# Performance work log

Measured on AMD Instinct MI355X. Metric: run time of the kernel, lower is better.

The kernel has to match this reference:

```python
import jax, jax.numpy as jnp
import numpy as np

N, E, D, L, G = 10000, 320000, 256, 5, 128
RWSE, DEG_V = 16, 1001
BN_EPS = 1e-5


def setup_inputs() -> dict:
    key = jax.random.key(0)
    ks = jax.random.split(key, 12)
    s = 1.0 / np.sqrt(D)
    return {
        'feat_id': jax.random.randint(ks[0], (N,), 0, 100000, dtype=jnp.int64 if jax.config.jax_enable_x64 else jnp.int32),
        'edge_index': jax.random.randint(ks[1], (2, E), 0, N),
        'batch_idx': jnp.sort(jax.random.randint(ks[2], (N,), 0, G)),
        'rwse': jax.random.normal(ks[3], (N, RWSE), jnp.float32),
        'in_degrees': jax.random.randint(ks[4], (N,), 0, DEG_V),
        # value_projection: Linear(fixed_input_dim=D -> D); stored as [in, out]
        'w_val': jax.random.normal(ks[5], (D, D), jnp.float32) * s,
        'b_val': jnp.zeros((D,), jnp.float32),
        # rwse_projection: Linear(RWSE -> D)
        'w_rwse': jax.random.normal(ks[6], (RWSE, D), jnp.float32) * (1.0 / np.sqrt(RWSE)),
        'b_rwse': jnp.zeros((D,), jnp.float32),
        # degree_embedding table (clamped to [0, 1000])
        'deg_emb': jax.random.normal(ks[7], (DEG_V, D), jnp.float32) * 0.02,
        # per-layer GIN MLP: Linear-ReLU-Linear, stacked over L layers
        'mlp_w1': jax.random.normal(ks[8], (L, D, D), jnp.float32) * s,
        'mlp_b1': jnp.zeros((L, D), jnp.float32),
        'mlp_w2': jax.random.normal(ks[9], (L, D, D), jnp.float32) * s,
        'mlp_b2': jnp.zeros((L, D), jnp.float32),
        # BatchNorm1d (eval mode: running stats)
        'bn_gamma': jnp.ones((L, D), jnp.float32),
        'bn_beta': jnp.zeros((L, D), jnp.float32),
        'bn_mean': jnp.zeros((L, D), jnp.float32),
        'bn_var': jax.random.uniform(ks[10], (L, D), jnp.float32, 0.5, 1.5),
        # GIN eps per layer
        'eps_gin': jnp.zeros((L,), jnp.float32),
    }


def reference(feat_id, edge_index, batch_idx, rwse, in_degrees,
              w_val, b_val, w_rwse, b_rwse, deg_emb,
              mlp_w1, mlp_b1, mlp_w2, mlp_b2,
              bn_gamma, bn_beta, bn_mean, bn_var, eps_gin):
    # --- node feature embedding ---
    h_id = jnp.remainder(feat_id, D)
    h_one = jax.nn.one_hot(h_id, D, dtype=jnp.float32)            # [N, D]
    h = h_one @ w_val + b_val + rwse @ w_rwse + b_rwse            # value + rwse projections
    deg = jnp.clip(in_degrees, 0, 1000)
    h = h + deg_emb[deg]                                          # degree embedding

    src, dst = edge_index[0], edge_index[1]
    for l in range(L):
        # GIN message passing: sum neighbor features into dst (gather -> scatter-add)
        agg = jax.ops.segment_sum(h[src], dst, num_segments=N)    # [N, D]
        y = agg + (1.0 + eps_gin[l]) * h
        # MLP (Linear-ReLU-Linear)
        y = jax.nn.relu(y @ mlp_w1[l] + mlp_b1[l]) @ mlp_w2[l] + mlp_b2[l]
        # BatchNorm1d (eval: running stats) + ReLU
        y = (y - bn_mean[l]) * (bn_gamma[l] * jax.lax.rsqrt(bn_var[l] + BN_EPS)) + bn_beta[l]
        h = jax.nn.relu(y)

    # --- mean pooling per graph ---
    sums = jax.ops.segment_sum(h, batch_idx, num_segments=G)                     # [G, D]
    cnt = jax.ops.segment_sum(jnp.ones((N, 1), h.dtype), batch_idx, num_segments=G)
    graph_feature = sums / jnp.maximum(cnt, 1.0)
    return graph_feature, h
```

## Files before the change

kernel.cpp:

```cpp
#include <hip/hip_runtime.h>
#include <hip/hip_bf16.h>

#define N_NODES 10000
#define N_EDGES 320000
#define DIM     256
#define N_LAYERS 5
#define N_GRAPHS 128
#define RWSE_K  16
#define GBM 16

typedef __bf16 bf16_t;
typedef bf16_t bf16x8 __attribute__((ext_vector_type(8)));
typedef float  f32x4  __attribute__((ext_vector_type(4)));

__device__ inline ushort f2bf(float f) {
    union { float f; unsigned u; } v; v.f = f;
    unsigned r = v.u + 0x7fff + ((v.u >> 16) & 1);
    return (ushort)(r >> 16);
}
__device__ inline float bfbits2f(unsigned hi16) {
    union { unsigned u; float f; } v; v.u = hi16;
    return v.f;
}

__global__ __launch_bounds__(256)
void setup_kernel(const int* __restrict__ feat_id,
                  const float* __restrict__ rwse,
                  const int* __restrict__ in_deg,
                  const float* __restrict__ w_val,
                  const float* __restrict__ b_val,
                  const float* __restrict__ w_rwse,
                  const float* __restrict__ b_rwse,
                  const float* __restrict__ deg_emb,
                  ushort* __restrict__ hb,
                  const int* __restrict__ ei, int* __restrict__ cnt_arr,
                  const float* __restrict__ w1, const float* __restrict__ w2,
                  ushort* __restrict__ wt1, ushort* __restrict__ wt2,
                  const float* __restrict__ gamma, const float* __restrict__ beta,
                  const float* __restrict__ mean, const float* __restrict__ var,
                  const float* __restrict__ b2, float* __restrict__ scale,
                  float* __restrict__ shift) {
    __shared__ float r[RWSE_K];
    __shared__ float t[32][33];
    int b = blockIdx.x;
    int tid = threadIdx.x;
    if (b < N_NODES) {
        int i = b, d = tid;
        if (d < RWSE_K) r[d] = rwse[i * RWSE_K + d];
        __syncthreads();
        int hid = feat_id[i] & (DIM - 1);
        int dg = in_deg[i];
        dg = dg < 0 ? 0 : (dg > 1000 ? 1000 : dg);
        float v = w_val[hid * DIM + d] + b_val[d] + b_rwse[d] + deg_emb[dg * DIM + d];
#pragma unroll
        for (int k = 0; k < RWSE_K; ++k) v += r[k] * w_rwse[k * DIM + d];
        hb[i * DIM + d] = f2bf(v);
    } else if (b < 11250) {
        int e = (b - N_NODES) * 256 + tid;
        if (e < N_EDGES) atomicAdd(&cnt_arr[ei[N_EDGES + e]], 1);
    } else if (b < 11890) {
        int w_id = b - 11250;
        int l = w_id >> 7;
        int rem = w_id & 127;
        int mat = rem >> 6;
        int tile = rem & 63;
        const float* W  = (mat ? w2  : w1)  + (size_t)l * DIM * DIM;
        ushort*      Wt = (mat ? wt2 : wt1) + (size_t)l * DIM * DIM;
        int k0 = (tile >> 3) * 32, n0 = (tile & 7) * 32;
        int tx = tid & 31, ty = tid >> 5;
#pragma unroll
        for (int j = 0; j < 4; ++j)
            t[ty + j * 8][tx] = W[(k0 + ty + j * 8) * DIM + n0 + tx];
        __syncthreads();
#pragma unroll
        for (int j = 0; j < 4; ++j)
            Wt[(n0 + ty + j * 8) * DIM + k0 + tx] = f2bf(t[tx][ty + j * 8]);
    } else {
        int l = b - 11890;
        int idx = l * DIM + tid;
        float s = gamma[idx] * rsqrtf(var[idx] + 1e-5f);
        scale[idx] = s;
        shift[idx] = beta[idx] + (b2[idx] - mean[idx]) * s;
    }
}

__global__ __launch_bounds__(1024)
void scan_kernel(const int* __restrict__ cnt_arr, int* __restrict__ cur, int n) {
    __shared__ int wsum[16];
    __shared__ int carry_sh;
    int tid = threadIdx.x, wave = tid >> 6, lane = tid & 63;
    if (tid == 0) carry_sh = 0;
    __syncthreads();
    for (int base = 0; base < n; base += 1024) {
        int idx = base + tid;
        int v = (idx < n) ? cnt_arr[idx] : 0;
        int s = v;
#pragma unroll
        for (int off = 1; off < 64; off <<= 1) {
            int t = __shfl_up(s, off, 64);
            if (lane >= off) s += t;
        }
        if (lane == 63) wsum[wave] = s;
        __syncthreads();
        if (wave == 0) {
            int ws = (lane < 16) ? wsum[lane] : 0;
#pragma unroll
            for (int off = 1; off < 16; off <<= 1) {
                int t = __shfl_up(ws, off, 64);
                if (lane >= off) ws += t;
            }
            if (lane < 16) wsum[lane] = ws;
        }
        __syncthreads();
        int excl = s - v + (wave ? wsum[wave - 1] : 0) + carry_sh;
        if (idx < n) cur[idx] = excl;
        __syncthreads();
        if (tid == 0) carry_sh += wsum[15];
        __syncthreads();
    }
}

__global__ __launch_bounds__(256)
void fill_kernel(const int* __restrict__ ei, int* __restrict__ cur,
                 int* __restrict__ cs) {
    int e = blockIdx.x * 256 + threadIdx.x;
    if (e < N_EDGES) {
        int d = ei[N_EDGES + e];
        int p = atomicAdd(&cur[d], 1);
        cs[p] = ei[e];
    }
}

#define ACCV(v)                                                        \
    acc[0] += bfbits2f((v).x << 16); acc[1] += bfbits2f((v).x & 0xffff0000u); \
    acc[2] += bfbits2f((v).y << 16); acc[3] += bfbits2f((v).y & 0xffff0000u); \
    acc[4] += bfbits2f((v).z << 16); acc[5] += bfbits2f((v).z & 0xffff0000u); \
    acc[6] += bfbits2f((v).w << 16); acc[7] += bfbits2f((v).w & 0xffff0000u);

__global__ __launch_bounds__(256)
void agg_kernel(const ushort* __restrict__ hb,
                const int* __restrict__ cur, const int* __restrict__ cs,
                const float* __restrict__ eps_gin, int layer,
                ushort* __restrict__ y) {
    int wave = threadIdx.x >> 6;
    int lane = threadIdx.x & 63;
    int half = lane >> 5;
    int sl   = lane & 31;
    int i = blockIdx.x * 4 + wave;
    if (i >= N_NODES) return;
    const uint4* hb4 = (const uint4*)hb;
    float acc[8];
#pragma unroll
    for (int t = 0; t < 8; ++t) acc[t] = 0.f;

    int e0 = i ? cur[i - 1] : 0;
    int e1 = cur[i];
    for (int base = e0; base < e1; base += 64) {
        int rem = e1 - base;
        int cnt = rem < 64 ? rem : 64;
        int idx = (base + lane < e1) ? cs[base + lane] : 0;
        int j = 0;
        for (; j + 8 <= cnt; j += 8) {
            int s0 = __shfl(idx, j + half, 64);
            int s1 = __shfl(idx, j + 2 + half, 64);
            int s2 = __shfl(idx, j + 4 + half, 64);
            int s3 = __shfl(idx, j + 6 + half, 64);
            uint4 v0 = hb4[(size_t)s0 * 32 + sl];
            uint4 v1 = hb4[(size_t)s1 * 32 + sl];
            uint4 v2 = hb4[(size_t)s2 * 32 + sl];
            uint4 v3 = hb4[(size_t)s3 * 32 + sl];
            ACCV(v0); ACCV(v1); ACCV(v2); ACCV(v3);
        }
        for (; j + 2 <= cnt; j += 2) {
            int s = __shfl(idx, j + half, 64);
            uint4 v = hb4[(size_t)s * 32 + sl];
            ACCV(v);
        }
        if (j < cnt) {
            int s = __shfl(idx, j, 64);
            if (half == 0) {
                uint4 v = hb4[(size_t)s * 32 + sl];
                ACCV(v);
            }
        }
    }
#pragma unroll
    for (int t = 0; t < 8; ++t) acc[t] += __shfl_xor(acc[t], 32, 64);
    if (half == 0) {
        float sc = 1.0f + eps_gin[layer];
        uint4 sv = hb4[(size_t)i * 32 + sl];
        acc[0] += bfbits2f(sv.x << 16) * sc; acc[1] += bfbits2f(sv.x & 0xffff0000u) * sc;
        acc[2] += bfbits2f(sv.y << 16) * sc; acc[3] += bfbits2f(sv.y & 0xffff0000u) * sc;
        acc[4] += bfbits2f(sv.z << 16) * sc; acc[5] += bfbits2f(sv.z & 0xffff0000u) * sc;
        acc[6] += bfbits2f(sv.w << 16) * sc; acc[7] += bfbits2f(sv.w & 0xffff0000u) * sc;
        uint4 o;
        o.x = (uint)f2bf(acc[0]) | ((uint)f2bf(acc[1]) << 16);
        o.y = (uint)f2bf(acc[2]) | ((uint)f2bf(acc[3]) << 16);
        o.z = (uint)f2bf(acc[4]) | ((uint)f2bf(acc[5]) << 16);
        o.w = (uint)f2bf(acc[6]) | ((uint)f2bf(acc[7]) << 16);
        ((uint4*)y)[(size_t)i * 32 + sl] = o;
    }
}

__global__ __launch_bounds__(256)
void gemm12_kernel(const ushort* __restrict__ A, const ushort* __restrict__ Wt1,
                   const float* __restrict__ b1, const ushort* __restrict__ Wt2,
                   const float* __restrict__ bnsc, const float* __restrict__ bnsh,
                   float* __restrict__ outF, ushort* __restrict__ outB, int nrows) {
    __shared__ __align__(16) ushort As[GBM][40];
    __shared__ __align__(16) ushort Bs[DIM][40];
    __shared__ __align__(16) ushort Ts[GBM][DIM + 8];
    int tx = threadIdx.x;
    int row0 = blockIdx.x * GBM;
    int wave = tx >> 6, lane = tx & 63, quad = lane >> 4, l16 = lane & 15;
    int wc = wave * 64;
    int srow = tx >> 2;
    int skol = (tx & 3) * 8;

    f32x4 acc[4];
#pragma unroll
    for (int t = 0; t < 4; ++t) acc[t] = (f32x4){0.f, 0.f, 0.f, 0.f};

    for (int k0 = 0; k0 < DIM; k0 += 32) {
        if (tx < 64) {
            int arow = row0 + srow;
            uint4 av = make_uint4(0u, 0u, 0u, 0u);
            if (arow < nrows) av = *(const uint4*)&A[(size_t)arow * DIM + k0 + skol];
            *(uint4*)&As[srow][skol] = av;
        }
#pragma unroll
        for (int j = 0; j < 4; ++j) {
            int r = srow + 64 * j;
            *(uint4*)&Bs[r][skol] = *(const uint4*)&Wt1[(size_t)r * DIM + k0 + skol];
        }
        __syncthreads();
        bf16x8 af = *(const bf16x8*)&As[l16][quad * 8];
#pragma unroll
        for (int tj = 0; tj < 4; ++tj) {
            bf16x8 bf = *(const bf16x8*)&Bs[wc + tj * 16 + l16][quad * 8];
            acc[tj] = __builtin_amdgcn_mfma_f32_16x16x32_bf16(af, bf, acc[tj], 0, 0, 0);
        }
        __syncthreads();
    }
#pragma unroll
    for (int tj = 0; tj < 4; ++tj) {
        int col = wc + tj * 16 + l16;
        float bias = b1[col];
#pragma unroll
        for (int r = 0; r < 4; ++r)
            Ts[quad * 4 + r][col] = f2bf(fmaxf(acc[tj][r] + bias, 0.f));
    }
    __syncthreads();

#pragma unroll
    for (int t = 0; t < 4; ++t) acc[t] = (f32x4){0.f, 0.f, 0.f, 0.f};
    for (int k0 = 0; k0 < DIM; k0 += 32) {
#pragma unroll
        for (int j = 0; j < 4; ++j) {
            int r = srow + 64 * j;
            *(uint4*)&Bs[r][skol] = *(const uint4*)&Wt2[(size_t)r * DIM + k0 + skol];
        }
        __syncthreads();
        bf16x8 af = *(const bf16x8*)&Ts[l16][k0 + quad * 8];
#pragma unroll
        for (int tj = 0; tj < 4; ++tj) {
            bf16x8 bf = *(const bf16x8*)&Bs[wc + tj * 16 + l16][quad * 8];
            acc[tj] = __builtin_amdgcn_mfma_f32_16x16x32_bf16(af, bf, acc[tj], 0, 0, 0);
        }
        __syncthreads();
    }
#pragma unroll
    for (int tj = 0; tj < 4; ++tj) {
        int col = wc + tj * 16 + l16;
        float s = bnsc[col], sh = bnsh[col];
#pragma unroll
        for (int r = 0; r < 4; ++r) {
            int row = row0 + quad * 4 + r;
            if (row < nrows) {
                float v = fmaxf(acc[tj][r] * s + sh, 0.f);
                if (outF) outF[(size_t)row * DIM + col] = v;
                if (outB) outB[(size_t)row * DIM + col] = f2bf(v);
            }
        }
    }
}

__global__ __launch_bounds__(256)
void pool_kernel(const float* __restrict__ hfin, const int* __restrict__ batch,
                 float* __restrict__ out) {
    int g = blockIdx.x;
    int d = threadIdx.x;
    int l = 0, r = N_NODES;
    while (l < r) { int m = (l + r) >> 1; if (batch[m] < g) l = m + 1; else r = m; }
    int lo = l;
    r = N_NODES;
    while (l < r) { int m = (l + r) >> 1; if (batch[m] < g + 1) l = m + 1; else r = m; }
    int hi = l;
    float a0 = 0.f, a1 = 0.f, a2 = 0.f, a3 = 0.f;
    int i = lo;
    for (; i + 4 <= hi; i += 4) {
        a0 += hfin[(size_t)i * DIM + d];
        a1 += hfin[(size_t)(i + 1) * DIM + d];
        a2 += hfin[(size_t)(i + 2) * DIM + d];
        a3 += hfin[(size_t)(i + 3) * DIM + d];
    }
    for (; i < hi; ++i) a0 += hfin[(size_t)i * DIM + d];
    float c = (float)(hi - lo);
    if (c < 1.f) c = 1.f;
    out[g * DIM + d] = ((a0 + a1) + (a2 + a3)) / c;
}

extern "C" void kernel_launch(void* const* d_in, const int* in_sizes, int n_in,
                              void* d_out, int out_size, void* d_ws, size_t ws_size,
                              hipStream_t stream) {
    const int*   feat_id  = (const int*)d_in[0];
    const int*   ei       = (const int*)d_in[1];
    const int*   batch    = (const int*)d_in[2];
    const float* rwse     = (const float*)d_in[3];
    const int*   in_deg   = (const int*)d_in[4];
    const float* w_val    = (const float*)d_in[5];
    const float* b_val    = (const float*)d_in[6];
    const float* w_rwse   = (const float*)d_in[7];
    const float* b_rwse   = (const float*)d_in[8];
    const float* deg_emb  = (const float*)d_in[9];
    const float* mlp_w1   = (const float*)d_in[10];
    const float* mlp_b1   = (const float*)d_in[11];
    const float* mlp_w2   = (const float*)d_in[12];
    const float* mlp_b2   = (const float*)d_in[13];
    const float* bn_gamma = (const float*)d_in[14];
    const float* bn_beta  = (const float*)d_in[15];
    const float* bn_mean  = (const float*)d_in[16];
    const float* bn_var   = (const float*)d_in[17];
    const float* eps_gin  = (const float*)d_in[18];

    float* out = (float*)d_out;
    float* out_h = out + N_GRAPHS * DIM;

    char* w = (char*)d_ws;
    ushort* hb   = (ushort*)w;
    ushort* y    = hb + (size_t)N_NODES * DIM;
    ushort* wt1  = y + (size_t)N_NODES * DIM;
    ushort* wt2  = wt1 + (size_t)N_LAYERS * DIM * DIM;
    int* cnt_arr = (int*)(wt2 + (size_t)N_LAYERS * DIM * DIM);
    int* cur     = cnt_arr + N_NODES;
    int* cs      = cur + N_NODES;
    float* bnsc  = (float*)(cs + N_EDGES);
    float* bnsh  = bnsc + N_LAYERS * DIM;

    hipMemsetAsync(cnt_arr, 0, N_NODES * sizeof(int), stream);

    setup_kernel<<<11895, 256, 0, stream>>>(
        feat_id, rwse, in_deg, w_val, b_val, w_rwse, b_rwse, deg_emb,
        hb, ei, cnt_arr, mlp_w1, mlp_w2, wt1, wt2,
        bn_gamma, bn_beta, bn_mean, bn_var, mlp_b2, bnsc, bnsh);
    scan_kernel<<<1, 1024, 0, stream>>>(cnt_arr, cur, N_NODES);
    fill_kernel<<<(N_EDGES + 255) / 256, 256, 0, stream>>>(ei, cur, cs);

    int agrid = (N_NODES + 3) / 4;
    int ggrid = (N_NODES + GBM - 1) / GBM;
    for (int l = 0; l < N_LAYERS; ++l) {
        agg_kernel<<<agrid, 256, 0, stream>>>(hb, cur, cs, eps_gin, l, y);
        bool last = (l == N_LAYERS - 1);
        gemm12_kernel<<<ggrid, 256, 0, stream>>>(
            y, wt1 + (size_t)l * DIM * DIM, mlp_b1 + l * DIM,
            wt2 + (size_t)l * DIM * DIM, bnsc + l * DIM, bnsh + l * DIM,
            last ? out_h : nullptr, last ? nullptr : hb, N_NODES);
    }

    pool_kernel<<<N_GRAPHS, 256, 0, stream>>>(out_h, batch, out);
}
```

Measured before the change: 342.0 us.

## Fuse neighbor aggregation into the per-layer MLP GEMM kernel with ping-pong buffers

Merges the gather/scatter aggregation and the two-layer MLP into a single per-layer kernel. Each block aggregates its 16 rows straight into shared memory, which removes the intermediate y buffer round trip through global memory and one launch per layer. Because a layer now reads h while writing the next h, two node-feature buffers alternate between layers. The catch is less parallelism in the gather phase: each wave handles 4 nodes in sequence, with fewer blocks in flight and more shared memory per block, which can lower occupancy.

Measured after the change: 329.7 us. -3.6%, faster.

```diff
diff --git a/kernel.cpp b/kernel.cpp
--- a/kernel.cpp
+++ b/kernel.cpp
@@ -138,107 +138,97 @@
     acc[6] += bfbits2f((v).w << 16); acc[7] += bfbits2f((v).w & 0xffff0000u);
 
 __global__ __launch_bounds__(256)
-void agg_kernel(const ushort* __restrict__ hb,
-                const int* __restrict__ cur, const int* __restrict__ cs,
-                const float* __restrict__ eps_gin, int layer,
-                ushort* __restrict__ y) {
-    int wave = threadIdx.x >> 6;
-    int lane = threadIdx.x & 63;
-    int half = lane >> 5;
-    int sl   = lane & 31;
-    int i = blockIdx.x * 4 + wave;
-    if (i >= N_NODES) return;
-    const uint4* hb4 = (const uint4*)hb;
-    float acc[8];
-#pragma unroll
-    for (int t = 0; t < 8; ++t) acc[t] = 0.f;
-
-    int e0 = i ? cur[i - 1] : 0;
-    int e1 = cur[i];
-    for (int base = e0; base < e1; base += 64) {
-        int rem = e1 - base;
-        int cnt = rem < 64 ? rem : 64;
-        int idx = (base + lane < e1) ? cs[base + lane] : 0;
-        int j = 0;
-        for (; j + 8 <= cnt; j += 8) {
-            int s0 = __shfl(idx, j + half, 64);
-            int s1 = __shfl(idx, j + 2 + half, 64);
-            int s2 = __shfl(idx, j + 4 + half, 64);
-            int s3 = __shfl(idx, j + 6 + half, 64);
-            uint4 v0 = hb4[(size_t)s0 * 32 + sl];
-            uint4 v1 = hb4[(size_t)s1 * 32 + sl];
-            uint4 v2 = hb4[(size_t)s2 * 32 + sl];
-            uint4 v3 = hb4[(size_t)s3 * 32 + sl];
-            ACCV(v0); ACCV(v1); ACCV(v2); ACCV(v3);
-        }
-        for (; j + 2 <= cnt; j += 2) {
-            int s = __shfl(idx, j + half, 64);
-            uint4 v = hb4[(size_t)s * 32 + sl];
-            ACCV(v);
-        }
-        if (j < cnt) {
-            int s = __shfl(idx, j, 64);
-            if (half == 0) {
-                uint4 v = hb4[(size_t)s * 32 + sl];
-                ACCV(v);
-            }
-        }
-    }
-#pragma unroll
-    for (int t = 0; t < 8; ++t) acc[t] += __shfl_xor(acc[t], 32, 64);
-    if (half == 0) {
-        float sc = 1.0f + eps_gin[layer];
-        uint4 sv = hb4[(size_t)i * 32 + sl];
-        acc[0] += bfbits2f(sv.x << 16) * sc; acc[1] += bfbits2f(sv.x & 0xffff0000u) * sc;
-        acc[2] += bfbits2f(sv.y << 16) * sc; acc[3] += bfbits2f(sv.y & 0xffff0000u) * sc;
-        acc[4] += bfbits2f(sv.z << 16) * sc; acc[5] += bfbits2f(sv.z & 0xffff0000u) * sc;
-        acc[6] += bfbits2f(sv.w << 16) * sc; acc[7] += bfbits2f(sv.w & 0xffff0000u) * sc;
-        uint4 o;
-        o.x = (uint)f2bf(acc[0]) | ((uint)f2bf(acc[1]) << 16);
-        o.y = (uint)f2bf(acc[2]) | ((uint)f2bf(acc[3]) << 16);
-        o.z = (uint)f2bf(acc[4]) | ((uint)f2bf(acc[5]) << 16);
-        o.w = (uint)f2bf(acc[6]) | ((uint)f2bf(acc[7]) << 16);
-        ((uint4*)y)[(size_t)i * 32 + sl] = o;
-    }
-}
-
-__global__ __launch_bounds__(256)
-void gemm12_kernel(const ushort* __restrict__ A, const ushort* __restrict__ Wt1,
-                   const float* __restrict__ b1, const ushort* __restrict__ Wt2,
-                   const float* __restrict__ bnsc, const float* __restrict__ bnsh,
-                   float* __restrict__ outF, ushort* __restrict__ outB, int nrows) {
-    __shared__ __align__(16) ushort As[GBM][40];
+void layer_kernel(const ushort* __restrict__ hb_in,
+                  const int* __restrict__ cur, const int* __restrict__ cs,
+                  const float* __restrict__ eps_gin, int layer,
+                  const ushort* __restrict__ Wt1, const float* __restrict__ b1,
+                  const ushort* __restrict__ Wt2,
+                  const float* __restrict__ bnsc, const float* __restrict__ bnsh,
+                  float* __restrict__ outF, ushort* __restrict__ outB) {
+    __shared__ __align__(16) ushort As[GBM][DIM + 8];
     __shared__ __align__(16) ushort Bs[DIM][40];
     __shared__ __align__(16) ushort Ts[GBM][DIM + 8];
     int tx = threadIdx.x;
     int row0 = blockIdx.x * GBM;
     int wave = tx >> 6, lane = tx & 63, quad = lane >> 4, l16 = lane & 15;
+    int half = lane >> 5, sl = lane & 31;
     int wc = wave * 64;
     int srow = tx >> 2;
     int skol = (tx & 3) * 8;
-
-    f32x4 acc[4];
-#pragma unroll
-    for (int t = 0; t < 4; ++t) acc[t] = (f32x4){0.f, 0.f, 0.f, 0.f};
-
+    const uint4* hb4 = (const uint4*)hb_in;
+    float sc = 1.0f + eps_gin[layer];
+
+#pragma unroll
+    for (int n = 0; n < 4; ++n) {
+        int r = wave * 4 + n;
+        int i = row0 + r;
+        float acc[8];
+#pragma unroll
+        for (int t = 0; t < 8; ++t) acc[t] = 0.f;
+        int e0 = i ? cur[i - 1] : 0;
+        int e1 = cur[i];
+        for (int base = e0; base < e1; base += 64) {
+            int rem = e1 - base;
+            int cnt = rem < 64 ? rem : 64;
+            int idx = (base + lane < e1) ? cs[base + lane] : 0;
+            int j = 0;
+            for (; j + 8 <= cnt; j += 8) {
+                int s0 = __shfl(idx, j + half, 64);
+                int s1 = __shfl(idx, j + 2 + half, 64);
+                int s2 = __shfl(idx, j + 4 + half, 64);
+                int s3 = __shfl(idx, j + 6 + half, 64);
+                uint4 v0 = hb4[(size_t)s0 * 32 + sl];
+                uint4 v1 = hb4[(size_t)s1 * 32 + sl];
+                uint4 v2 = hb4[(size_t)s2 * 32 + sl];
+                uint4 v3 = hb4[(size_t)s3 * 32 + sl];
+                ACCV(v0); ACCV(v1); ACCV(v2); ACCV(v3);
+            }
+            for (; j + 2 <= cnt; j += 2) {
+                int s = __shfl(idx, j + half, 64);
+                uint4 v = hb4[(size_t)s * 32 + sl];
+                ACCV(v);
+            }
+            if (j < cnt) {
+                int s = __shfl(idx, j, 64);
+                if (half == 0) {
+                    uint4 v = hb4[(size_t)s * 32 + sl];
+                    ACCV(v);
+                }
+            }
+        }
+#pragma unroll
+        for (int t = 0; t < 8; ++t) acc[t] += __shfl_xor(acc[t], 32, 64);
+        if (half == 0) {
+            uint4 sv = hb4[(size_t)i * 32 + sl];
+            acc[0] += bfbits2f(sv.x << 16) * sc; acc[1] += bfbits2f(sv.x & 0xffff0000u) * sc;
+            acc[2] += bfbits2f(sv.y << 16) * sc; acc[3] += bfbits2f(sv.y & 0xffff0000u) * sc;
+            acc[4] += bfbits2f(sv.z << 16) * sc; acc[5] += bfbits2f(sv.z & 0xffff0000u) * sc;
+            acc[6] += bfbits2f(sv.w << 16) * sc; acc[7] += bfbits2f(sv.w & 0xffff0000u) * sc;
+            uint4 o;
+            o.x = (uint)f2bf(acc[0]) | ((uint)f2bf(acc[1]) << 16);
+            o.y = (uint)f2bf(acc[2]) | ((uint)f2bf(acc[3]) << 16);
+            o.z = (uint)f2bf(acc[4]) | ((uint)f2bf(acc[5]) << 16);
+            o.w = (uint)f2bf(acc[6]) | ((uint)f2bf(acc[7]) << 16);
+            *(uint4*)&As[r][sl * 8] = o;
+        }
+    }
+    __syncthreads();
+
+    f32x4 acc4[4];
+#pragma unroll
+    for (int t = 0; t < 4; ++t) acc4[t] = (f32x4){0.f, 0.f, 0.f, 0.f};
     for (int k0 = 0; k0 < DIM; k0 += 32) {
-        if (tx < 64) {
-            int arow = row0 + srow;
-            uint4 av = make_uint4(0u, 0u, 0u, 0u);
-            if (arow < nrows) av = *(const uint4*)&A[(size_t)arow * DIM + k0 + skol];
-            *(uint4*)&As[srow][skol] = av;
-        }
 #pragma unroll
         for (int j = 0; j < 4; ++j) {
-            int r = srow + 64 * j;
-            *(uint4*)&Bs[r][skol] = *(const uint4*)&Wt1[(size_t)r * DIM + k0 + skol];
-        }
-        __syncthreads();
-        bf16x8 af = *(const bf16x8*)&As[l16][quad * 8];
+            int rr = srow + 64 * j;
+            *(uint4*)&Bs[rr][skol] = *(const uint4*)&Wt1[(size_t)rr * DIM + k0 + skol];
+        }
+        __syncthreads();
+        bf16x8 af = *(const bf16x8*)&As[l16][k0 + quad * 8];
 #pragma unroll
         for (int tj = 0; tj < 4; ++tj) {
-            bf16x8 bf = *(const bf16x8*)&Bs[wc + tj * 16 + l16][quad * 8];
-            acc[tj] = __builtin_amdgcn_mfma_f32_16x16x32_bf16(af, bf, acc[tj], 0, 0, 0);
+            bf16x8 bfv = *(const bf16x8*)&Bs[wc + tj * 16 + l16][quad * 8];
+            acc4[tj] = __builtin_amdgcn_mfma_f32_16x16x32_bf16(af, bfv, acc4[tj], 0, 0, 0);
         }
         __syncthreads();
     }
@@ -248,24 +238,24 @@
         float bias = b1[col];
 #pragma unroll
         for (int r = 0; r < 4; ++r)
-            Ts[quad * 4 + r][col] = f2bf(fmaxf(acc[tj][r] + bias, 0.f));
+            Ts[quad * 4 + r][col] = f2bf(fmaxf(acc4[tj][r] + bias, 0.f));
     }
     __syncthreads();
 
 #pragma unroll
-    for (int t = 0; t < 4; ++t) acc[t] = (f32x4){0.f, 0.f, 0.f, 0.f};
+    for (int t = 0; t < 4; ++t) acc4[t] = (f32x4){0.f, 0.f, 0.f, 0.f};
     for (int k0 = 0; k0 < DIM; k0 += 32) {
 #pragma unroll
         for (int j = 0; j < 4; ++j) {
-            int r = srow + 64 * j;
-            *(uint4*)&Bs[r][skol] = *(const uint4*)&Wt2[(size_t)r * DIM + k0 + skol];
+            int rr = srow + 64 * j;
+            *(uint4*)&Bs[rr][skol] = *(const uint4*)&Wt2[(size_t)rr * DIM + k0 + skol];
         }
         __syncthreads();
         bf16x8 af = *(const bf16x8*)&Ts[l16][k0 + quad * 8];
 #pragma unroll
         for (int tj = 0; tj < 4; ++tj) {
-            bf16x8 bf = *(const bf16x8*)&Bs[wc + tj * 16 + l16][quad * 8];
-            acc[tj] = __builtin_amdgcn_mfma_f32_16x16x32_bf16(af, bf, acc[tj], 0, 0, 0);
+            bf16x8 bfv = *(const bf16x8*)&Bs[wc + tj * 16 + l16][quad * 8];
+            acc4[tj] = __builtin_amdgcn_mfma_f32_16x16x32_bf16(af, bfv, acc4[tj], 0, 0, 0);
         }
         __syncthreads();
     }
@@ -276,11 +266,9 @@
 #pragma unroll
         for (int r = 0; r < 4; ++r) {
             int row = row0 + quad * 4 + r;
-            if (row < nrows) {
-                float v = fmaxf(acc[tj][r] * s + sh, 0.f);
-                if (outF) outF[(size_t)row * DIM + col] = v;
-                if (outB) outB[(size_t)row * DIM + col] = f2bf(v);
-            }
+            float v = fmaxf(acc4[tj][r] * s + sh, 0.f);
+            if (outF) outF[(size_t)row * DIM + col] = v;
+            if (outB) outB[(size_t)row * DIM + col] = f2bf(v);
         }
     }
 }
@@ -337,9 +325,9 @@
     float* out_h = out + N_GRAPHS * DIM;
 
     char* w = (char*)d_ws;
-    ushort* hb   = (ushort*)w;
-    ushort* y    = hb + (size_t)N_NODES * DIM;
-    ushort* wt1  = y + (size_t)N_NODES * DIM;
+    ushort* hb0  = (ushort*)w;
+    ushort* hb1  = hb0 + (size_t)N_NODES * DIM;
+    ushort* wt1  = hb1 + (size_t)N_NODES * DIM;
     ushort* wt2  = wt1 + (size_t)N_LAYERS * DIM * DIM;
     int* cnt_arr = (int*)(wt2 + (size_t)N_LAYERS * DIM * DIM);
     int* cur     = cnt_arr + N_NODES;
@@ -351,20 +339,21 @@
 
     setup_kernel<<<11895, 256, 0, stream>>>(
         feat_id, rwse, in_deg, w_val, b_val, w_rwse, b_rwse, deg_emb,
-        hb, ei, cnt_arr, mlp_w1, mlp_w2, wt1, wt2,
+        hb0, ei, cnt_arr, mlp_w1, mlp_w2, wt1, wt2,
         bn_gamma, bn_beta, bn_mean, bn_var, mlp_b2, bnsc, bnsh);
     scan_kernel<<<1, 1024, 0, stream>>>(cnt_arr, cur, N_NODES);
     fill_kernel<<<(N_EDGES + 255) / 256, 256, 0, stream>>>(ei, cur, cs);
 
-    int agrid = (N_NODES + 3) / 4;
-    int ggrid = (N_NODES + GBM - 1) / GBM;
+    int ggrid = N_NODES / GBM;
     for (int l = 0; l < N_LAYERS; ++l) {
-        agg_kernel<<<agrid, 256, 0, stream>>>(hb, cur, cs, eps_gin, l, y);
         bool last = (l == N_LAYERS - 1);
-        gemm12_kernel<<<ggrid, 256, 0, stream>>>(
-            y, wt1 + (size_t)l * DIM * DIM, mlp_b1 + l * DIM,
+        const ushort* hin = (l & 1) ? hb1 : hb0;
+        ushort* hout = (l & 1) ? hb0 : hb1;
+        layer_kernel<<<ggrid, 256, 0, stream>>>(
+            hin, cur, cs, eps_gin, l,
+            wt1 + (size_t)l * DIM * DIM, mlp_b1 + l * DIM,
             wt2 + (size_t)l * DIM * DIM, bnsc + l * DIM, bnsh + l * DIM,
-            last ? out_h : nullptr, last ? nullptr : hb, N_NODES);
+            last ? out_h : nullptr, last ? nullptr : hout);
     }
 
     pool_kernel<<<N_GRAPHS, 256, 0, stream>>>(out_h, batch, out);
```
